# Optimization experiments

Measured on AMD Instinct MI355X. Metric: run time of the kernel, lower is better.

## Reference

```python
import jax, jax.numpy as jnp
import numpy as np

B, INP, OUP, FGROUP, H, W = 32, 256, 256, 8, 64, 64
CG = INP // FGROUP  # channels per group in GLGF fc1 layers


def conv3x3(x, w):
    # x: (N,1,H,W), w: (1,1,3,3); stride 1, padding 1 (SAME)
    return jax.lax.conv_general_dilated(
        x, w, window_strides=(1, 1), padding='SAME',
        dimension_numbers=('NCHW', 'OIHW', 'NCHW'))


def setup_inputs() -> dict:
    key = jax.random.key(0)
    ks = jax.random.split(key, 8)
    return {
        'x': jax.random.normal(ks[0], (B, INP, H, W), dtype=jnp.float32),
        # GLGF params (all 1x1 convs, bias=False), stored as dense matrices
        'w1l': jax.random.normal(ks[1], (FGROUP, CG, CG), dtype=jnp.float32) * 0.05,   # wn_fc1_l (groups=fgroup)
        'w1g1': jax.random.normal(ks[2], (FGROUP, CG), dtype=jnp.float32) * 0.05,      # wn_fc1_g1 (inp->fgroup, groups=fgroup)
        'w1g2': jax.random.normal(ks[3], (INP, FGROUP), dtype=jnp.float32) * 0.05,     # wn_fc1_g2 (fgroup->inp dense)
        'w2l': jax.random.normal(ks[4], (INP, OUP), dtype=jnp.float32) * 0.05,         # wn_fc2_l (groups=inp): input ch i -> oup outputs
        'w2g': jax.random.normal(ks[5], (INP,), dtype=jnp.float32) * 0.05,             # wn_fc2_g (inp->1 dense)
        'conv1_w': jax.random.normal(ks[6], (1, 1, 3, 3), dtype=jnp.float32) * 0.1,
        'conv2_w': jax.random.normal(ks[7], (1, 1, 3, 3), dtype=jnp.float32) * 0.1,
    }


def reference(x, w1l, w1g1, w1g2, w2l, w2g, conv1_w, conv2_w):
    b, c, h, w_ = x.shape
    fgroup, cg, _ = w1l.shape
    oup = w2l.shape[1]

    # adaptive_avg_pool2d(x, (1,1)) -> (B, inp) descriptor
    g = x.mean(axis=(2, 3))                                   # (B, inp)
    gg = g.reshape(b, fgroup, cg)

    # GLGF: fc1_l (grouped) + fc1_g2(fc1_g1) (squeeze to fgroup then expand)
    local = jnp.einsum('bgi,goi->bgo', gg, w1l).reshape(b, c)  # (B, inp)
    glob = jnp.einsum('bgi,gi->bg', gg, w1g1) @ w1g2.T         # (B, inp)
    s = jax.nn.sigmoid(local + glob)                           # (B, inp)

    # fc2_l (groups=inp): torch channel order is (input_ch g, out j) -> g*oup + j
    # fc2_g adds a per-sample scalar to every channel
    xw = s[:, :, None] * w2l + (s @ w2g)[:, None, None]        # (B, inp, oup)
    # WA_1Conv reinterprets the flat (oup*inp) channels as (oup, inp)
    Wdyn = xw.reshape(b, oup, c)                               # (B, oup, inp)

    # grouped conv with groups=batch, ksize=1 == per-sample matmul
    y = jnp.einsum('bihw,boi->bohw', x, Wdyn)                  # (B, oup, H, W)

    # channel gating: mean over channels -> conv3x3 -> sigmoid -> conv3x3
    cmap = y.mean(axis=1, keepdims=True)                       # (B, 1, H, W)
    cmap = conv3x3(cmap, conv1_w)
    cmap = jax.nn.sigmoid(cmap)
    cmap = conv3x3(cmap, conv2_w)
    return y * cmap
```

## Files before the change

kernel.cpp:

```cpp
#include <hip/hip_runtime.h>
#include <hip/hip_bf16.h>

typedef float  f32x4  __attribute__((ext_vector_type(4)));
typedef short  bf16x8 __attribute__((ext_vector_type(8)));

__device__ __forceinline__ short f2bf(float f) {
    union { __hip_bfloat16 h; short s; } u;
    u.h = __float2bfloat16(f);
    return u.s;
}

__device__ __forceinline__ void gload_lds16(const void* g, void* l) {
    __builtin_amdgcn_global_load_lds(
        (const __attribute__((address_space(1))) unsigned int*)g,
        (__attribute__((address_space(3))) unsigned int*)l, 16, 0, 0);
}

__global__ __launch_bounds__(256) void transpose_kernel(const float* __restrict__ x,
                                                        short* __restrict__ xt,
                                                        float* __restrict__ gpart,
                                                        float* __restrict__ xsump) {
    const int pchunk = blockIdx.x;
    const int cchunk = blockIdx.y;
    const int c0 = cchunk * 64;
    const int b  = blockIdx.z;
    const int tid = threadIdx.x;
    const int cpair = tid >> 3;
    const int poct  = tid & 7;
    const int p0 = pchunk * 64;

    __shared__ unsigned int tile[64 * 32];

    const float* rowA = x + ((size_t)(b * 256 + c0 + 2 * cpair)) * 4096 + p0 + poct * 8;
    const float* rowB = rowA + 4096;
    float av[8], bv[8];
    *reinterpret_cast<float4*>(&av[0]) = *reinterpret_cast<const float4*>(rowA);
    *reinterpret_cast<float4*>(&av[4]) = *reinterpret_cast<const float4*>(rowA + 4);
    *reinterpret_cast<float4*>(&bv[0]) = *reinterpret_cast<const float4*>(rowB);
    *reinterpret_cast<float4*>(&bv[4]) = *reinterpret_cast<const float4*>(rowB + 4);

    float sA = 0.f, sB = 0.f;
    #pragma unroll
    for (int e = 0; e < 8; ++e) { sA += av[e]; sB += bv[e]; }
    sA += __shfl_xor(sA, 1, 64); sA += __shfl_xor(sA, 2, 64); sA += __shfl_xor(sA, 4, 64);
    sB += __shfl_xor(sB, 1, 64); sB += __shfl_xor(sB, 2, 64); sB += __shfl_xor(sB, 4, 64);
    if (poct == 0) {
        gpart[((size_t)(b * 256 + c0 + 2 * cpair)) * 64 + pchunk] = sA;
        gpart[((size_t)(b * 256 + c0 + 2 * cpair + 1)) * 64 + pchunk] = sB;
    }

    float xs[8];
    #pragma unroll
    for (int e = 0; e < 8; ++e) {
        float v = av[e] + bv[e];
        v += __shfl_xor(v, 8, 64);
        v += __shfl_xor(v, 16, 64);
        v += __shfl_xor(v, 32, 64);
        xs[e] = v;
    }
    if ((tid & 56) == 0) {
        int wv = tid >> 6;
        float* dst = xsump + ((size_t)((cchunk * 4 + wv) * 32 + b)) * 4096 + p0 + poct * 8;
        *reinterpret_cast<f32x4*>(dst)     = *reinterpret_cast<f32x4*>(&xs[0]);
        *reinterpret_cast<f32x4*>(dst + 4) = *reinterpret_cast<f32x4*>(&xs[4]);
    }

    const int s = cpair >> 2, w = cpair & 3;
    #pragma unroll
    for (int e = 0; e < 8; ++e) {
        int p = poct * 8 + e;
        unsigned int u = (unsigned int)(unsigned short)f2bf(av[e]) |
                         ((unsigned int)(unsigned short)f2bf(bv[e]) << 16);
        tile[p * 32 + ((s ^ poct) << 2) + w] = u;
    }
    __syncthreads();

    const int so = tid & 7;
    #pragma unroll
    for (int h = 0; h < 2; ++h) {
        int p = (tid >> 3) + h * 32;
        int sp = so ^ ((p >> 3) & 7);
        uint4 v = *reinterpret_cast<const uint4*>(&tile[p * 32 + sp * 4]);
        *reinterpret_cast<uint4*>(xt + ((size_t)b * 4096 + p0 + p) * 256 + c0 + so * 8) = v;
    }
}

__global__ __launch_bounds__(256) void prep_kernel(
    const float* __restrict__ gpart, const float* __restrict__ w1l,
    const float* __restrict__ w1g1, const float* __restrict__ w1g2,
    const float* __restrict__ w2l, const float* __restrict__ w2g,
    float* __restrict__ s_out, float* __restrict__ t_out,
    float* __restrict__ vq_out, short* __restrict__ w2l_bf) {
    int b = blockIdx.x;
    int tid = threadIdx.x;
    if (b >= 32) {
        int seg = b - 32;
        const float* src = w2l + seg * 4096;
        short* dst = w2l_bf + seg * 4096;
        #pragma unroll
        for (int it = 0; it < 4; ++it) {
            float4 v = *reinterpret_cast<const float4*>(src + it * 1024 + tid * 4);
            short4 o;
            o.x = f2bf(v.x); o.y = f2bf(v.y); o.z = f2bf(v.z); o.w = f2bf(v.w);
            *reinterpret_cast<short4*>(dst + it * 1024 + tid * 4) = o;
        }
        return;
    }
    __shared__ float gs[256];
    __shared__ float zs[8];
    __shared__ float ss[256];
    __shared__ float red[4];
    {
        const float4* gp = reinterpret_cast<const float4*>(gpart + (size_t)(b * 256 + tid) * 64);
        float acc = 0.f;
        #pragma unroll
        for (int j = 0; j < 16; ++j) { float4 v = gp[j]; acc += v.x + v.y + v.z + v.w; }
        gs[tid] = acc * (1.0f / 4096.0f);
    }
    __syncthreads();
    if (tid < 8) {
        float z = 0.f;
        for (int i = 0; i < 32; ++i) z += gs[tid * 32 + i] * w1g1[tid * 32 + i];
        zs[tid] = z;
    }
    __syncthreads();
    int grp = tid >> 5, o = tid & 31;
    float local = 0.f;
    #pragma unroll 4
    for (int i = 0; i < 32; ++i) local += gs[grp * 32 + i] * w1l[grp * 1024 + o * 32 + i];
    float glob = 0.f;
    #pragma unroll
    for (int gg = 0; gg < 8; ++gg) glob += zs[gg] * w1g2[tid * 8 + gg];
    float sv = 1.0f / (1.0f + expf(-(local + glob)));
    ss[tid] = sv;
    s_out[b * 256 + tid] = sv;
    float tv = sv * w2g[tid];
    #pragma unroll
    for (int off = 32; off; off >>= 1) tv += __shfl_down(tv, off, 64);
    if ((tid & 63) == 0) red[tid >> 6] = tv;
    __syncthreads();
    float tb = red[0] + red[1] + red[2] + red[3];
    if (tid == 0) t_out[b] = tb;
    float v = 0.f;
    for (int o2 = 0; o2 < 256; ++o2) v += ss[o2] * w2l[o2 * 256 + tid];
    vq_out[b * 256 + tid] = v * (1.0f / 256.0f);
}

__global__ __launch_bounds__(256) void cmap0_kernel(const short* __restrict__ xt,
                                                    const float* __restrict__ vq,
                                                    const float* __restrict__ t,
                                                    const float* __restrict__ xsump,
                                                    float* __restrict__ cmap0,
                                                    float* __restrict__ txs) {
    const int b = blockIdx.y;
    const int p = blockIdx.x * 256 + threadIdx.x;
    __shared__ float vs[256];
    vs[threadIdx.x] = vq[b * 256 + threadIdx.x];
    __syncthreads();
    const uint4* row = reinterpret_cast<const uint4*>(xt + ((size_t)b * 4096 + p) * 256);
    float acc = 0.f;
    #pragma unroll 8
    for (int it = 0; it < 32; ++it) {
        uint4 u = row[it];
        const unsigned int* uw = reinterpret_cast<const unsigned int*>(&u);
        #pragma unroll
        for (int j = 0; j < 4; ++j) {
            unsigned int wrd = uw[j];
            union { unsigned int u; float f; } lo, hi;
            lo.u = wrd << 16;
            hi.u = wrd & 0xffff0000u;
            acc += lo.f * vs[it * 8 + 2 * j] + hi.f * vs[it * 8 + 2 * j + 1];
        }
    }
    float xs = 0.f;
    #pragma unroll
    for (int part = 0; part < 16; ++part)
        xs += xsump[((size_t)(part * 32 + b)) * 4096 + p];
    float tb = t[b];
    float tx = tb * xs;
    cmap0[b * 4096 + p] = acc + tx;
    txs[b * 4096 + p] = tx;
}

__global__ __launch_bounds__(256) void convs_kernel(const float* __restrict__ cmap0,
                                                    const float* __restrict__ w9a,
                                                    const float* __restrict__ w9b,
                                                    float* __restrict__ cmap) {
    const int strip = blockIdx.x;
    const int b = blockIdx.y;
    const int tid = threadIdx.x;
    const int r0 = strip * 16;
    const int rlo = (r0 == 0) ? 0 : r0 - 1;
    const int rhi = (r0 + 16 > 63) ? 63 : r0 + 16;
    const int cnt = rhi - rlo + 1;

    __shared__ float mid[18 * 64];
    float wa[9], wb[9];
    #pragma unroll
    for (int i = 0; i < 9; ++i) { wa[i] = w9a[i]; wb[i] = w9b[i]; }
    const float* ib = cmap0 + (size_t)b * 4096;

    for (int idx = tid; idx < cnt * 64; idx += 256) {
        int r = rlo + (idx >> 6), cc = idx & 63;
        float acc = 0.f;
        #pragma unroll
        for (int dy = -1; dy <= 1; ++dy)
            #pragma unroll
            for (int dx = -1; dx <= 1; ++dx) {
                int rr = r + dy, xx = cc + dx;
                if (rr >= 0 && rr < 64 && xx >= 0 && xx < 64)
                    acc += ib[rr * 64 + xx] * wa[(dy + 1) * 3 + (dx + 1)];
            }
        mid[idx] = 1.0f / (1.0f + expf(-acc));
    }
    __syncthreads();
    for (int idx = tid; idx < 1024; idx += 256) {
        int r = r0 + (idx >> 6), cc = idx & 63;
        float acc = 0.f;
        #pragma unroll
        for (int dy = -1; dy <= 1; ++dy)
            #pragma unroll
            for (int dx = -1; dx <= 1; ++dx) {
                int rr = r + dy, xx = cc + dx;
                if (rr >= 0 && rr < 64 && xx >= 0 && xx < 64)
                    acc += mid[(rr - rlo) * 64 + xx] * wb[(dy + 1) * 3 + (dx + 1)];
            }
        cmap[(size_t)b * 4096 + r * 64 + cc] = acc;
    }
}

__global__ __launch_bounds__(512) void gemm_epi_kernel(
    const short* __restrict__ xt, const short* __restrict__ w2l_bf,
    const float* __restrict__ s, const float* __restrict__ txs,
    const float* __restrict__ cmap, float* __restrict__ out) {
    const int b  = blockIdx.z;
    const int p0 = blockIdx.x * 64;
    const int tid  = threadIdx.x;
    const int lane = tid & 63;
    const int w    = tid >> 6;
    const int wm = w >> 1, wn = w & 1;

    __shared__ short Alds[256 * 64];
    __shared__ short Xlds[64 * 64];

    const int sl   = (lane & 7) ^ (lane >> 3);
    const int lrow = lane >> 3;

    f32x4 acc[4][2] = {};

    for (int ks = 0; ks < 256; ks += 64) {
        #pragma unroll
        for (int j = 0; j < 4; ++j) {
            int chunk = w * 4 + j;
            int row = chunk * 8 + lrow;
            gload_lds16(w2l_bf + (size_t)row * 256 + ks + sl * 8,
                        (char*)Alds + chunk * 1024);
        }
        {
            int prow = w * 8 + lrow;
            gload_lds16(xt + ((size_t)b * 4096 + p0 + prow) * 256 + ks + sl * 8,
                        (char*)Xlds + w * 1024);
        }
        __syncthreads();
        #pragma unroll
        for (int kk = 0; kk < 2; ++kk) {
            bf16x8 af[4], bfr[2];
            const int ss = kk * 4 + (lane >> 4);
            #pragma unroll
            for (int m = 0; m < 4; ++m) {
                int o = wm * 64 + m * 16 + (lane & 15);
                af[m] = *reinterpret_cast<const bf16x8*>(
                    (char*)Alds + o * 128 + ((ss ^ (lane & 7)) * 16));
            }
            #pragma unroll
            for (int n = 0; n < 2; ++n) {
                int p = wn * 32 + n * 16 + (lane & 15);
                bfr[n] = *reinterpret_cast<const bf16x8*>(
                    (char*)Xlds + p * 128 + ((ss ^ (lane & 7)) * 16));
            }
            #pragma unroll
            for (int m = 0; m < 4; ++m)
                #pragma unroll
                for (int n = 0; n < 2; ++n)
                    acc[m][n] = __builtin_amdgcn_mfma_f32_16x16x32_bf16(af[m], bfr[n], acc[m][n], 0, 0, 0);
        }
        __syncthreads();
    }
    #pragma unroll
    for (int n = 0; n < 2; ++n) {
        int p = p0 + wn * 32 + n * 16 + (lane & 15);
        float tx = txs[b * 4096 + p];
        float cm = cmap[b * 4096 + p];
        #pragma unroll
        for (int m = 0; m < 4; ++m) {
            #pragma unroll
            for (int r = 0; r < 4; ++r) {
                int o = wm * 64 + m * 16 + (lane >> 4) * 4 + r;
                float yv = s[b * 256 + o] * acc[m][n][r] + tx;
                out[((size_t)b * 256 + o) * 4096 + p] = yv * cm;
            }
        }
    }
}

extern "C" void kernel_launch(void* const* d_in, const int* in_sizes, int n_in,
                              void* d_out, int out_size, void* d_ws, size_t ws_size,
                              hipStream_t stream) {
    const float* x       = (const float*)d_in[0];
    const float* w1l     = (const float*)d_in[1];
    const float* w1g1    = (const float*)d_in[2];
    const float* w1g2    = (const float*)d_in[3];
    const float* w2l     = (const float*)d_in[4];
    const float* w2g     = (const float*)d_in[5];
    const float* conv1_w = (const float*)d_in[6];
    const float* conv2_w = (const float*)d_in[7];
    float* out = (float*)d_out;

    float* wsf    = (float*)d_ws;
    float* s      = wsf;
    float* t      = wsf + 8192;
    float* vq     = wsf + 8256;
    float* cmap0  = wsf + 16448;
    float* txs    = wsf + 147520;
    float* cmap   = wsf + 278592;
    float* gpart  = wsf + 409664;
    float* xsump  = wsf + 933952;
    short* w2l_bf = (short*)(wsf + 3031104);
    short* xt     = (short*)(wsf + 3063872);

    transpose_kernel<<<dim3(64, 4, 32), 256, 0, stream>>>(x, xt, gpart, xsump);
    prep_kernel<<<48, 256, 0, stream>>>(gpart, w1l, w1g1, w1g2, w2l, w2g, s, t, vq, w2l_bf);
    cmap0_kernel<<<dim3(16, 32), 256, 0, stream>>>(xt, vq, t, xsump, cmap0, txs);
    convs_kernel<<<dim3(4, 32), 256, 0, stream>>>(cmap0, conv1_w, conv2_w, cmap);
    gemm_epi_kernel<<<dim3(64, 1, 32), 512, 0, stream>>>(xt, w2l_bf, s, txs, cmap, out);
}
```

Baseline: 129.6 us.

## Fuse cmap0 into conv kernel and retile GEMM to 128x128 with vector stores

Merges the channel-mean projection into the 3x3 conv kernel, recomputing a two-row halo per 16-row strip so the cmap0 buffer and one launch go away. The GEMM is retiled to 128 output channels by 128 pixels per 256-thread block. Its MFMA operands are swapped so each lane holds four consecutive pixels, which lets the epilogue issue 16-byte vectorized loads and stores. The costs are fewer blocks (128) doing the heavy projection with redundant halo rows, plus reloading xt for each of the two output-channel halves.

```diff
diff --git a/kernel.cpp b/kernel.cpp
--- a/kernel.cpp
+++ b/kernel.cpp
@@ -146,62 +146,61 @@
     vq_out[b * 256 + tid] = v * (1.0f / 256.0f);
 }
 
-__global__ __launch_bounds__(256) void cmap0_kernel(const short* __restrict__ xt,
-                                                    const float* __restrict__ vq,
-                                                    const float* __restrict__ t,
-                                                    const float* __restrict__ xsump,
-                                                    float* __restrict__ cmap0,
-                                                    float* __restrict__ txs) {
-    const int b = blockIdx.y;
-    const int p = blockIdx.x * 256 + threadIdx.x;
-    __shared__ float vs[256];
-    vs[threadIdx.x] = vq[b * 256 + threadIdx.x];
-    __syncthreads();
-    const uint4* row = reinterpret_cast<const uint4*>(xt + ((size_t)b * 4096 + p) * 256);
-    float acc = 0.f;
-    #pragma unroll 8
-    for (int it = 0; it < 32; ++it) {
-        uint4 u = row[it];
-        const unsigned int* uw = reinterpret_cast<const unsigned int*>(&u);
-        #pragma unroll
-        for (int j = 0; j < 4; ++j) {
-            unsigned int wrd = uw[j];
-            union { unsigned int u; float f; } lo, hi;
-            lo.u = wrd << 16;
-            hi.u = wrd & 0xffff0000u;
-            acc += lo.f * vs[it * 8 + 2 * j] + hi.f * vs[it * 8 + 2 * j + 1];
-        }
-    }
-    float xs = 0.f;
-    #pragma unroll
-    for (int part = 0; part < 16; ++part)
-        xs += xsump[((size_t)(part * 32 + b)) * 4096 + p];
-    float tb = t[b];
-    float tx = tb * xs;
-    cmap0[b * 4096 + p] = acc + tx;
-    txs[b * 4096 + p] = tx;
-}
-
-__global__ __launch_bounds__(256) void convs_kernel(const float* __restrict__ cmap0,
-                                                    const float* __restrict__ w9a,
-                                                    const float* __restrict__ w9b,
-                                                    float* __restrict__ cmap) {
+__global__ __launch_bounds__(256) void fused_cmap_kernel(
+    const short* __restrict__ xt, const float* __restrict__ vq,
+    const float* __restrict__ t, const float* __restrict__ xsump,
+    const float* __restrict__ w9a, const float* __restrict__ w9b,
+    float* __restrict__ txs, float* __restrict__ cmap) {
     const int strip = blockIdx.x;
     const int b = blockIdx.y;
     const int tid = threadIdx.x;
     const int r0 = strip * 16;
-    const int rlo = (r0 == 0) ? 0 : r0 - 1;
-    const int rhi = (r0 + 16 > 63) ? 63 : r0 + 16;
-    const int cnt = rhi - rlo + 1;
-
+    const int rlo2 = (r0 >= 2) ? r0 - 2 : 0;
+    const int rhi2 = (r0 + 17 <= 63) ? r0 + 17 : 63;
+    const int n2 = rhi2 - rlo2 + 1;
+    const int rlo1 = (r0 >= 1) ? r0 - 1 : 0;
+    const int rhi1 = (r0 + 16 <= 63) ? r0 + 16 : 63;
+    const int n1 = rhi1 - rlo1 + 1;
+
+    __shared__ float c0[20 * 64];
     __shared__ float mid[18 * 64];
+    __shared__ float vs[256];
+    vs[tid] = vq[b * 256 + tid];
     float wa[9], wb[9];
     #pragma unroll
     for (int i = 0; i < 9; ++i) { wa[i] = w9a[i]; wb[i] = w9b[i]; }
-    const float* ib = cmap0 + (size_t)b * 4096;
-
-    for (int idx = tid; idx < cnt * 64; idx += 256) {
-        int r = rlo + (idx >> 6), cc = idx & 63;
+    const float tb = t[b];
+    __syncthreads();
+
+    for (int idx = tid; idx < n2 * 64; idx += 256) {
+        int r = rlo2 + (idx >> 6);
+        int p = r * 64 + (idx & 63);
+        const uint4* row = reinterpret_cast<const uint4*>(xt + ((size_t)b * 4096 + p) * 256);
+        float acc = 0.f;
+        #pragma unroll 8
+        for (int it = 0; it < 32; ++it) {
+            uint4 u = row[it];
+            const unsigned int* uw = reinterpret_cast<const unsigned int*>(&u);
+            #pragma unroll
+            for (int j = 0; j < 4; ++j) {
+                unsigned int wrd = uw[j];
+                union { unsigned int u; float f; } lo, hi;
+                lo.u = wrd << 16;
+                hi.u = wrd & 0xffff0000u;
+                acc += lo.f * vs[it * 8 + 2 * j] + hi.f * vs[it * 8 + 2 * j + 1];
+            }
+        }
+        float xs = 0.f;
+        #pragma unroll
+        for (int part = 0; part < 16; ++part)
+            xs += xsump[((size_t)(part * 32 + b)) * 4096 + p];
+        float tx = tb * xs;
+        c0[idx] = acc + tx;
+        if (r >= r0 && r < r0 + 16) txs[(size_t)b * 4096 + p] = tx;
+    }
+    __syncthreads();
+    for (int idx = tid; idx < n1 * 64; idx += 256) {
+        int r = rlo1 + (idx >> 6), cc = idx & 63;
         float acc = 0.f;
         #pragma unroll
         for (int dy = -1; dy <= 1; ++dy)
@@ -209,7 +208,7 @@
             for (int dx = -1; dx <= 1; ++dx) {
                 int rr = r + dy, xx = cc + dx;
                 if (rr >= 0 && rr < 64 && xx >= 0 && xx < 64)
-                    acc += ib[rr * 64 + xx] * wa[(dy + 1) * 3 + (dx + 1)];
+                    acc += c0[(rr - rlo2) * 64 + xx] * wa[(dy + 1) * 3 + (dx + 1)];
             }
         mid[idx] = 1.0f / (1.0f + expf(-acc));
     }
@@ -223,82 +222,79 @@
             for (int dx = -1; dx <= 1; ++dx) {
                 int rr = r + dy, xx = cc + dx;
                 if (rr >= 0 && rr < 64 && xx >= 0 && xx < 64)
-                    acc += mid[(rr - rlo) * 64 + xx] * wb[(dy + 1) * 3 + (dx + 1)];
+                    acc += mid[(rr - rlo1) * 64 + xx] * wb[(dy + 1) * 3 + (dx + 1)];
             }
         cmap[(size_t)b * 4096 + r * 64 + cc] = acc;
     }
 }
 
-__global__ __launch_bounds__(512) void gemm_epi_kernel(
+__global__ __launch_bounds__(256) void gemm_epi_kernel(
     const short* __restrict__ xt, const short* __restrict__ w2l_bf,
     const float* __restrict__ s, const float* __restrict__ txs,
     const float* __restrict__ cmap, float* __restrict__ out) {
     const int b  = blockIdx.z;
-    const int p0 = blockIdx.x * 64;
+    const int p0 = blockIdx.x * 128;
+    const int o0 = blockIdx.y * 128;
     const int tid  = threadIdx.x;
     const int lane = tid & 63;
     const int w    = tid >> 6;
     const int wm = w >> 1, wn = w & 1;
 
-    __shared__ short Alds[256 * 64];
-    __shared__ short Xlds[64 * 64];
+    __shared__ short Alds[128 * 64];
+    __shared__ short Xlds[128 * 64];
 
     const int sl   = (lane & 7) ^ (lane >> 3);
     const int lrow = lane >> 3;
 
-    f32x4 acc[4][2] = {};
+    f32x4 acc[4][4] = {};
 
     for (int ks = 0; ks < 256; ks += 64) {
         #pragma unroll
         for (int j = 0; j < 4; ++j) {
-            int chunk = w * 4 + j;
-            int row = chunk * 8 + lrow;
-            gload_lds16(w2l_bf + (size_t)row * 256 + ks + sl * 8,
-                        (char*)Alds + chunk * 1024);
-        }
-        {
-            int prow = w * 8 + lrow;
-            gload_lds16(xt + ((size_t)b * 4096 + p0 + prow) * 256 + ks + sl * 8,
-                        (char*)Xlds + w * 1024);
+            int row = j * 32 + w * 8 + lrow;
+            gload_lds16(w2l_bf + (size_t)(o0 + row) * 256 + ks + sl * 8,
+                        (char*)Alds + (j * 32 + w * 8) * 128);
+            gload_lds16(xt + ((size_t)b * 4096 + p0 + row) * 256 + ks + sl * 8,
+                        (char*)Xlds + (j * 32 + w * 8) * 128);
         }
         __syncthreads();
         #pragma unroll
         for (int kk = 0; kk < 2; ++kk) {
-            bf16x8 af[4], bfr[2];
+            bf16x8 af[4], xf[4];
             const int ss = kk * 4 + (lane >> 4);
             #pragma unroll
             for (int m = 0; m < 4; ++m) {
                 int o = wm * 64 + m * 16 + (lane & 15);
                 af[m] = *reinterpret_cast<const bf16x8*>(
                     (char*)Alds + o * 128 + ((ss ^ (lane & 7)) * 16));
-            }
-            #pragma unroll
-            for (int n = 0; n < 2; ++n) {
-                int p = wn * 32 + n * 16 + (lane & 15);
-                bfr[n] = *reinterpret_cast<const bf16x8*>(
+                int p = wn * 64 + m * 16 + (lane & 15);
+                xf[m] = *reinterpret_cast<const bf16x8*>(
                     (char*)Xlds + p * 128 + ((ss ^ (lane & 7)) * 16));
             }
             #pragma unroll
             for (int m = 0; m < 4; ++m)
                 #pragma unroll
-                for (int n = 0; n < 2; ++n)
-                    acc[m][n] = __builtin_amdgcn_mfma_f32_16x16x32_bf16(af[m], bfr[n], acc[m][n], 0, 0, 0);
+                for (int n = 0; n < 4; ++n)
+                    acc[m][n] = __builtin_amdgcn_mfma_f32_16x16x32_bf16(xf[n], af[m], acc[m][n], 0, 0, 0);
         }
         __syncthreads();
     }
-    #pragma unroll
-    for (int n = 0; n < 2; ++n) {
-        int p = p0 + wn * 32 + n * 16 + (lane & 15);
-        float tx = txs[b * 4096 + p];
-        float cm = cmap[b * 4096 + p];
+    float sv[4];
+    #pragma unroll
+    for (int m = 0; m < 4; ++m)
+        sv[m] = s[b * 256 + o0 + wm * 64 + m * 16 + (lane & 15)];
+    #pragma unroll
+    for (int n = 0; n < 4; ++n) {
+        int pb = p0 + wn * 64 + n * 16 + (lane >> 4) * 4;
+        f32x4 tx4 = *reinterpret_cast<const f32x4*>(txs + (size_t)b * 4096 + pb);
+        f32x4 cm4 = *reinterpret_cast<const f32x4*>(cmap + (size_t)b * 4096 + pb);
         #pragma unroll
         for (int m = 0; m < 4; ++m) {
-            #pragma unroll
-            for (int r = 0; r < 4; ++r) {
-                int o = wm * 64 + m * 16 + (lane >> 4) * 4 + r;
-                float yv = s[b * 256 + o] * acc[m][n][r] + tx;
-                out[((size_t)b * 256 + o) * 4096 + p] = yv * cm;
-            }
+            int o = o0 + wm * 64 + m * 16 + (lane & 15);
+            f32x4 y;
+            #pragma unroll
+            for (int r = 0; r < 4; ++r) y[r] = (sv[m] * acc[m][n][r] + tx4[r]) * cm4[r];
+            *reinterpret_cast<f32x4*>(out + ((size_t)b * 256 + o) * 4096 + pb) = y;
         }
     }
 }
@@ -320,17 +316,15 @@
     float* s      = wsf;
     float* t      = wsf + 8192;
     float* vq     = wsf + 8256;
-    float* cmap0  = wsf + 16448;
-    float* txs    = wsf + 147520;
-    float* cmap   = wsf + 278592;
-    float* gpart  = wsf + 409664;
-    float* xsump  = wsf + 933952;
-    short* w2l_bf = (short*)(wsf + 3031104);
-    short* xt     = (short*)(wsf + 3063872);
+    float* txs    = wsf + 16448;
+    float* cmap   = wsf + 147520;
+    float* gpart  = wsf + 278592;
+    float* xsump  = wsf + 802880;
+    short* w2l_bf = (short*)(wsf + 2900032);
+    short* xt     = (short*)(wsf + 2932800);
 
     transpose_kernel<<<dim3(64, 4, 32), 256, 0, stream>>>(x, xt, gpart, xsump);
     prep_kernel<<<48, 256, 0, stream>>>(gpart, w1l, w1g1, w1g2, w2l, w2g, s, t, vq, w2l_bf);
-    cmap0_kernel<<<dim3(16, 32), 256, 0, stream>>>(xt, vq, t, xsump, cmap0, txs);
-    convs_kernel<<<dim3(4, 32), 256, 0, stream>>>(cmap0, conv1_w, conv2_w, cmap);
-    gemm_epi_kernel<<<dim3(64, 1, 32), 512, 0, stream>>>(xt, w2l_bf, s, txs, cmap, out);
-}
+    fused_cmap_kernel<<<dim3(4, 32), 256, 0, stream>>>(xt, vq, t, xsump, conv1_w, conv2_w, txs, cmap);
+    gemm_epi_kernel<<<dim3(32, 2, 32), 256, 0, stream>>>(xt, w2l_bf, s, txs, cmap, out);
+}
```

New measurement: 142.8 us. +10.3%, slower.

## Double-buffer GEMM LDS staging and pre-reduce channel sums in transpose

Applied to the files above, without the earlier changes.

The GEMM kernel now uses two LDS buffers. Global-to-LDS loads for the next K slice are issued before computing the current one, with explicit vmcnt waits and raw barriers in place of __syncthreads. The transpose kernel also reduces its four per-wave channel partial sums in shared memory before writing. This cuts xsump writes and cmap0 reads from 16 partials to 4 and shrinks the workspace layout. The cost is double the GEMM LDS (about 80KB per block), which may lower occupancy, and correctness now relies on hand-written waitcnt counts.

```diff
diff --git a/kernel.cpp b/kernel.cpp
--- a/kernel.cpp
+++ b/kernel.cpp
@@ -30,6 +30,7 @@
     const int p0 = pchunk * 64;
 
     __shared__ unsigned int tile[64 * 32];
+    __shared__ float xred[4 * 64];
 
     const float* rowA = x + ((size_t)(b * 256 + c0 + 2 * cpair)) * 4096 + p0 + poct * 8;
     const float* rowB = rowA + 4096;
@@ -60,9 +61,8 @@
     }
     if ((tid & 56) == 0) {
         int wv = tid >> 6;
-        float* dst = xsump + ((size_t)((cchunk * 4 + wv) * 32 + b)) * 4096 + p0 + poct * 8;
-        *reinterpret_cast<f32x4*>(dst)     = *reinterpret_cast<f32x4*>(&xs[0]);
-        *reinterpret_cast<f32x4*>(dst + 4) = *reinterpret_cast<f32x4*>(&xs[4]);
+        #pragma unroll
+        for (int e = 0; e < 8; ++e) xred[wv * 64 + poct * 8 + e] = xs[e];
     }
 
     const int s = cpair >> 2, w = cpair & 3;
@@ -74,6 +74,11 @@
         tile[p * 32 + ((s ^ poct) << 2) + w] = u;
     }
     __syncthreads();
+
+    if (tid < 64) {
+        float v = xred[tid] + xred[64 + tid] + xred[128 + tid] + xred[192 + tid];
+        xsump[((size_t)(cchunk * 32 + b)) * 4096 + p0 + tid] = v;
+    }
 
     const int so = tid & 7;
     #pragma unroll
@@ -174,7 +179,7 @@
     }
     float xs = 0.f;
     #pragma unroll
-    for (int part = 0; part < 16; ++part)
+    for (int part = 0; part < 4; ++part)
         xs += xsump[((size_t)(part * 32 + b)) * 4096 + p];
     float tb = t[b];
     float tx = tb * xs;
@@ -240,28 +245,39 @@
     const int w    = tid >> 6;
     const int wm = w >> 1, wn = w & 1;
 
-    __shared__ short Alds[256 * 64];
-    __shared__ short Xlds[64 * 64];
+    __shared__ short Alds[2][256 * 64];
+    __shared__ short Xlds[2][64 * 64];
 
     const int sl   = (lane & 7) ^ (lane >> 3);
     const int lrow = lane >> 3;
 
     f32x4 acc[4][2] = {};
 
-    for (int ks = 0; ks < 256; ks += 64) {
+    auto STAGE = [&](int bi, int ks) {
         #pragma unroll
         for (int j = 0; j < 4; ++j) {
             int chunk = w * 4 + j;
             int row = chunk * 8 + lrow;
             gload_lds16(w2l_bf + (size_t)row * 256 + ks + sl * 8,
-                        (char*)Alds + chunk * 1024);
-        }
-        {
-            int prow = w * 8 + lrow;
-            gload_lds16(xt + ((size_t)b * 4096 + p0 + prow) * 256 + ks + sl * 8,
-                        (char*)Xlds + w * 1024);
-        }
-        __syncthreads();
+                        (char*)(&Alds[bi][0]) + chunk * 1024);
+        }
+        int prow = w * 8 + lrow;
+        gload_lds16(xt + ((size_t)b * 4096 + p0 + prow) * 256 + ks + sl * 8,
+                    (char*)(&Xlds[bi][0]) + w * 1024);
+    };
+
+    STAGE(0, 0);
+    #pragma unroll
+    for (int t = 0; t < 4; ++t) {
+        const int bi = t & 1;
+        if (t < 3) {
+            STAGE(bi ^ 1, (t + 1) * 64);
+            asm volatile("s_waitcnt vmcnt(5)" ::: "memory");
+        } else {
+            asm volatile("s_waitcnt vmcnt(0)" ::: "memory");
+        }
+        __builtin_amdgcn_s_barrier();
+        asm volatile("" ::: "memory");
         #pragma unroll
         for (int kk = 0; kk < 2; ++kk) {
             bf16x8 af[4], bfr[2];
@@ -270,13 +286,13 @@
             for (int m = 0; m < 4; ++m) {
                 int o = wm * 64 + m * 16 + (lane & 15);
                 af[m] = *reinterpret_cast<const bf16x8*>(
-                    (char*)Alds + o * 128 + ((ss ^ (lane & 7)) * 16));
+                    (char*)(&Alds[bi][0]) + o * 128 + ((ss ^ (lane & 7)) * 16));
             }
             #pragma unroll
             for (int n = 0; n < 2; ++n) {
                 int p = wn * 32 + n * 16 + (lane & 15);
                 bfr[n] = *reinterpret_cast<const bf16x8*>(
-                    (char*)Xlds + p * 128 + ((ss ^ (lane & 7)) * 16));
+                    (char*)(&Xlds[bi][0]) + p * 128 + ((ss ^ (lane & 7)) * 16));
             }
             #pragma unroll
             for (int m = 0; m < 4; ++m)
@@ -284,7 +300,8 @@
                 for (int n = 0; n < 2; ++n)
                     acc[m][n] = __builtin_amdgcn_mfma_f32_16x16x32_bf16(af[m], bfr[n], acc[m][n], 0, 0, 0);
         }
-        __syncthreads();
+        asm volatile("" ::: "memory");
+        __builtin_amdgcn_s_barrier();
     }
     #pragma unroll
     for (int n = 0; n < 2; ++n) {
@@ -325,8 +342,8 @@
     float* cmap   = wsf + 278592;
     float* gpart  = wsf + 409664;
     float* xsump  = wsf + 933952;
-    short* w2l_bf = (short*)(wsf + 3031104);
-    short* xt     = (short*)(wsf + 3063872);
+    short* w2l_bf = (short*)(wsf + 1458240);
+    short* xt     = (short*)(wsf + 1491008);
 
     transpose_kernel<<<dim3(64, 4, 32), 256, 0, stream>>>(x, xt, gpart, xsump);
     prep_kernel<<<48, 256, 0, stream>>>(gpart, w1l, w1g1, w1g2, w2l, w2g, s, t, vq, w2l_bf);
```

Measured after the change: 125.5 us. 3.1% less time.
